# Kernel optimization log

Hardware: AMD Instinct MI355X
Metric: run time of the kernel (lower is better)

The kernel has to match this reference:

```python
import jax, jax.numpy as jnp
import numpy as np

THRESH = 0.5
LENS = 0.5
DECAY = 0.5
IN_SIZE = 8
T = 784 // IN_SIZE  # 98 timesteps
H = 1024
OUT = 10
SKIP = (2, 3, 4)
N_BATCH = 1024


@jax.custom_vjp
def act_fun(x):
    return (x > THRESH).astype(x.dtype)

def _af_fwd(x):
    return act_fun(x), x

def _af_bwd(x, g):
    return (g * (jnp.abs(x - THRESH) < LENS).astype(g.dtype),)

act_fun.defvjp(_af_fwd, _af_bwd)


def _make_mask(dim, cycle):
    base = np.array([1 if t % cycle == 0 else 0 for t in range(T)], dtype=np.int32)
    return np.stack([np.roll(base, n) for n in range(dim)])  # [dim, T]


def setup_inputs() -> dict:
    key = jax.random.key(0)
    ks = jax.random.split(key, 9)
    inp = {
        "input": jax.random.uniform(ks[0], (N_BATCH, 784), dtype=jnp.float32),
        "W1": jax.random.normal(ks[1], (H, IN_SIZE), dtype=jnp.float32) * 0.1,
        "b1": jax.random.normal(ks[2], (H,), dtype=jnp.float32) * 0.01,
        "W2": jax.random.normal(ks[3], (H, H), dtype=jnp.float32) * 0.03,
        "b2": jax.random.normal(ks[4], (H,), dtype=jnp.float32) * 0.01,
        "W3": jax.random.normal(ks[5], (H, H), dtype=jnp.float32) * 0.03,
        "b3": jax.random.normal(ks[6], (H,), dtype=jnp.float32) * 0.01,
        "W4": jax.random.normal(ks[7], (OUT, H), dtype=jnp.float32) * 0.03,
        "b4": jax.random.normal(ks[8], (OUT,), dtype=jnp.float32) * 0.01,
        "mask1": jnp.asarray(_make_mask(H, SKIP[0])),
        "mask2": jnp.asarray(_make_mask(H, SKIP[1])),
        "mask3": jnp.asarray(_make_mask(H, SKIP[2])),
    }
    return inp


def _gather_steps(x):
    # Faithful replication of the original (buggy) slicing: start = step*IN_SIZE,
    # but if start >= T - IN_SIZE the model uses the LAST IN_SIZE pixels.
    starts = np.array([s * IN_SIZE if s * IN_SIZE < T - IN_SIZE else 784 - IN_SIZE
                       for s in range(T)])
    idx = starts[:, None] + np.arange(IN_SIZE)  # [T, IN_SIZE]
    return jnp.transpose(x[:, idx], (1, 0, 2))  # [T, N, IN_SIZE]


def reference(input, W1, b1, W2, b2, W3, b3, W4, b4, mask1, mask2, mask3):
    N = input.shape[0]
    xs = _gather_steps(input)            # [T, N, IN_SIZE]
    mk1 = mask1.T                         # [T, H]
    mk2 = mask2.T
    mk3 = mask3.T

    def upd(drive, mem, spike, mk):
        mkf = mk.astype(mem.dtype)
        new_mem = mem * DECAY * (1.0 - spike) + drive
        mem = jnp.where(mk == 0, mem, new_mem)
        spike = act_fun(mem) * mkf
        return mem, spike

    zeros = lambda d: jnp.zeros((N, d), dtype=input.dtype)
    carry0 = (zeros(H), zeros(H), zeros(H), zeros(H), zeros(H), zeros(H),
              jnp.zeros((N, OUT), dtype=input.dtype), zeros(H), zeros(H), zeros(H))

    def step(carry, inp):
        m1, s1, m2, s2, m3, s3, osum, ss1, ss2, ss3 = carry
        x, k1, k2, k3 = inp
        m1, s1 = upd(x @ W1.T + b1, m1, s1, k1)
        m2, s2 = upd(s1 @ W2.T + b2, m2, s2, k2)
        m3, s3 = upd(s2 @ W3.T + b3, m3, s3, k3)
        out = s3 @ W4.T + b4
        return (m1, s1, m2, s2, m3, s3, osum + out,
                ss1 + s1, ss2 + s2, ss3 + s3), None

    carry, _ = jax.lax.scan(step, carry0, (xs, mk1, mk2, mk3))
    _, _, _, _, _, _, osum, ss1, ss2, ss3 = carry

    tw = jnp.asarray(T, dtype=input.dtype)
    outputs = osum / tw
    denom = jnp.asarray(N * H * T, dtype=input.dtype)
    layer_fr = jnp.stack([ss1.sum() / denom, ss2.sum() / denom, ss3.sum() / denom])
    hidden_spk = (ss1 / tw, ss2 / tw, ss3 / tw)
    return outputs, hidden_spk, layer_fr
```

## Files before the change

kernel.cpp:

```cpp
#include <hip/hip_runtime.h>

#define TTL 98
#define OUTD 10

typedef float f16v __attribute__((ext_vector_type(16)));
typedef short short8 __attribute__((ext_vector_type(8)));
typedef unsigned long ul2 __attribute__((ext_vector_type(2)));
typedef unsigned short ushort;

constexpr size_t MM = 1048576;
constexpr size_t OFF_OSUM = 5 * MM;
constexpr size_t OFF_XT   = OFF_OSUM + 10240;
constexpr size_t OFF_S1B  = OFF_XT + 802816;
constexpr size_t OFF_S2B  = OFF_S1B + 1605632;
constexpr size_t OFF_S1BT = OFF_S2B + 1103872;
constexpr size_t OFF_S2BT = OFF_S1BT + 1605632;
constexpr size_t OFF_W2S  = OFF_S2BT + 1103872;
constexpr size_t OFF_W3S  = OFF_W2S + 1572864;
constexpr size_t FIX_END  = OFF_W3S + 1585152;

constexpr size_t TAB_IDX2 = 0;
constexpr size_t TAB_IDX3 = 37632;
constexpr size_t TAB_RK2  = 68992;
constexpr size_t TAB_RK3  = 169344;
constexpr size_t TAB_CQ3  = 269696;
constexpr size_t TAB_L2   = 304192;
constexpr size_t TAB_L3   = 337984;

__device__ inline void split3(float w, ushort& h, ushort& m, ushort& l) {
    unsigned u = __float_as_uint(w);
    h = (ushort)(u >> 16);
    float r1 = w - __uint_as_float(u & 0xFFFF0000u);
    unsigned u1 = __float_as_uint(r1);
    m = (ushort)(u1 >> 16);
    float r2 = r1 - __uint_as_float(u1 & 0xFFFF0000u);
    l = (ushort)(__float_as_uint(r2) >> 16);
}

__device__ inline short8 expand8(unsigned x) {
    union { unsigned u[4]; short8 v; } r;
#pragma unroll
    for (int q = 0; q < 4; ++q) {
        unsigned b = x >> (2 * q);
        r.u[q] = ((b & 1u) * 0x3F80u) | ((b & 2u) ? 0x3F800000u : 0u);
    }
    return r.v;
}

__global__ __launch_bounds__(256) void kSplit(
    const float* __restrict__ W2, const float* __restrict__ W3,
    ushort* __restrict__ W2S, ushort* __restrict__ W3S)
{
    int id = blockIdx.x * 256 + threadIdx.x;
    if (id < 1048576) {
        int p = id >> 19, rem = id & 524287, i = rem >> 9, q = rem & 511;
        ushort h, m, l;
        split3(W2[i * 1024 + 2 * q + p], h, m, l);
        size_t base = (size_t)p * 524288 + (size_t)i * 512 + q;
        W2S[base] = h; W2S[base + 1048576] = m; W2S[base + 2097152] = l;
    } else {
        int id2 = id - 1048576;
        if (id2 >= 1056768) return;
        int c = id2 / 352256, rem = id2 % 352256, i = rem / 344, q = rem % 344;
        int j = c + 3 * q;
        float w = (j < 1024) ? W3[i * 1024 + j] : 0.f;
        ushort h, m, l;
        split3(w, h, m, l);
        W3S[id2] = h; W3S[id2 + 1056768] = m; W3S[id2 + 2113536] = l;
    }
}

__global__ __launch_bounds__(256) void kPrep(const float* __restrict__ input,
                                             float* __restrict__ xT)
{
    __shared__ float Ls[64][65];
    int bx = blockIdx.x, tid = threadIdx.x;
    int wt = bx >> 4, nt = bx & 15;
    int w0 = wt * 64, n0 = nt * 64;
#pragma unroll
    for (int j = 0; j < 16; ++j) {
        int flat = tid + 256 * j;
        int a = flat >> 6, c = flat & 63;
        Ls[a][c] = (w0 + c < 784) ? input[(size_t)(n0 + a) * 784 + w0 + c] : 0.f;
    }
    __syncthreads();
#pragma unroll
    for (int j = 0; j < 16; ++j) {
        int flat = tid + 256 * j;
        int ii = flat >> 6, nn = flat & 63;
        if (w0 + ii < 784) xT[(size_t)(w0 + ii) * 1024 + n0 + nn] = Ls[nn][ii];
    }
}

__global__ __launch_bounds__(256) void kL1(
    const float* __restrict__ xT, const float* __restrict__ W1,
    const float* __restrict__ b1,
    unsigned long long* __restrict__ s1bits, float* __restrict__ ss1)
{
    int tid = threadIdx.x;
    int waveId = (blockIdx.x << 2) + (tid >> 6);
    int lane = tid & 63;
    int rowg = waveId >> 4;
    int nblk = waveId & 15;
    int i0 = rowg << 2;
    int n = (nblk << 6) + lane;
    float w[4][8], bb[4], mem[4], cnt[4];
#pragma unroll
    for (int r = 0; r < 4; ++r) {
#pragma unroll
        for (int e = 0; e < 8; ++e) w[r][e] = W1[(i0 + r) * 8 + e];
        bb[r] = b1[i0 + r]; mem[r] = 0.f; cnt[r] = 0.f;
    }
    float x[8], xn[8];
#pragma unroll
    for (int e = 0; e < 8; ++e) x[e] = xT[(size_t)e * 1024 + n];
    for (int t = 0; t < TTL; ++t) {
        if (t + 1 < TTL) {
            int st1 = ((t + 1) * 8 < TTL - 8) ? (t + 1) * 8 : (784 - 8);
#pragma unroll
            for (int e = 0; e < 8; ++e) xn[e] = xT[(size_t)(st1 + e) * 1024 + n];
        }
#pragma unroll
        for (int r = 0; r < 4; ++r) {
            if (((t ^ (i0 + r)) & 1) == 0) {
                float d = bb[r];
#pragma unroll
                for (int e = 0; e < 8; ++e) d += w[r][e] * x[e];
                float m = mem[r] * 0.5f + d;
                mem[r] = m;
                bool sp = m > 0.5f;
                unsigned long long bm = __ballot(sp);
                if (lane == 0) s1bits[(size_t)(t * 512 + ((i0 + r) >> 1)) * 16 + nblk] = bm;
                if (sp) cnt[r] += 1.f;
            }
        }
#pragma unroll
        for (int e = 0; e < 8; ++e) x[e] = xn[e];
    }
#pragma unroll
    for (int r = 0; r < 4; ++r) ss1[(size_t)(i0 + r) * 1024 + n] = cnt[r];
}

__global__ __launch_bounds__(256) void kTab2(
    int* __restrict__ idx2, int* __restrict__ idx3,
    int* __restrict__ rank2, int* __restrict__ rank3, int* __restrict__ cq3)
{
    __shared__ int f2[256], f3[256];
    __shared__ int sidx2[384], sidx3[320];
    int t = blockIdx.x, tid = threadIdx.x;
    int a2[4], a3[4];
    int l2 = 0, l3 = 0;
#pragma unroll
    for (int e = 0; e < 4; ++e) {
        int i = tid * 4 + e;
        int u = (t - i) % TTL; if (u < 0) u += TTL;
        a2[e] = (u % 3 == 0); a3[e] = (u % 4 == 0);
        l2 += a2[e]; l3 += a3[e];
    }
    f2[tid] = l2; f3[tid] = l3;
    __syncthreads();
    for (int s = 1; s < 256; s <<= 1) {
        int v2 = (tid >= s) ? f2[tid - s] : 0;
        int v3 = (tid >= s) ? f3[tid - s] : 0;
        __syncthreads();
        f2[tid] += v2; f3[tid] += v3;
        __syncthreads();
    }
    int o2 = f2[tid] - l2, o3 = f3[tid] - l3;
    int c2 = f2[255], c3 = f3[255];
#pragma unroll
    for (int e = 0; e < 4; ++e) {
        int i = tid * 4 + e;
        if (a2[e]) { rank2[t * 1024 + i] = o2; sidx2[o2] = i; ++o2; }
        else rank2[t * 1024 + i] = -1;
        if (a3[e]) { rank3[t * 1024 + i] = o3; sidx3[o3] = i; ++o3; }
        else rank3[t * 1024 + i] = -1;
    }
    __syncthreads();
    for (int k = tid; k < 384; k += 256) idx2[t * 384 + k] = (k < c2) ? sidx2[k] : -1;
    for (int k = tid; k < 320; k += 256) idx3[t * 320 + k] = (k < c3) ? sidx3[k] : -1;
    for (int k = tid; k < 352; k += 256) {
        int j = (k < c2) ? sidx2[k] : 0;
        cq3[t * 352 + k] = (j % 3) * 352256 + j / 3;
    }
}

__global__ __launch_bounds__(256) void kList(
    const int* __restrict__ rank2, const int* __restrict__ rank3,
    int* __restrict__ list2, int* __restrict__ list3)
{
    int i = blockIdx.x * 256 + threadIdx.x;
    int s2 = 0, s3 = 0;
    for (int t = 0; t < TTL; ++t) {
        int rk2 = rank2[t * 1024 + i];
        if (rk2 >= 0) list2[i * 33 + s2++] = (t << 10) | rk2;
        int rk3 = rank3[t * 1024 + i];
        if (rk3 >= 0) list3[i * 25 + s3++] = (t << 10) | rk3;
    }
}

template<int K>
__global__ __launch_bounds__(256) void kXb(const unsigned* __restrict__ in,
                                           unsigned* __restrict__ out, int t0)
{
    constexpr int Kw = K / 32;
    __shared__ unsigned L[1024];
    int bx = blockIdx.x, tid = threadIdx.x;
    int tt = t0 + bx / Kw, kw = bx % Kw;
    const unsigned* ip = in + ((size_t)tt * K + kw * 32) * 32;
#pragma unroll
    for (int g = 0; g < 4; ++g) L[g * 256 + tid] = ip[g * 256 + tid];
    __syncthreads();
    unsigned* op = out + ((size_t)tt * Kw + kw) * 1024;
#pragma unroll
    for (int g = 0; g < 4; ++g) {
        int n = g * 256 + tid;
        int w = n >> 5, b = n & 31;
        unsigned acc = 0;
#pragma unroll
        for (int k = 0; k < 32; ++k) acc |= ((L[k * 32 + w] >> b) & 1u) << k;
        op[n] = acc;
    }
}

__global__ __launch_bounds__(256) void kG3A(
    const ushort* __restrict__ Ws, const int* __restrict__ idx3,
    const int* __restrict__ cq3, ushort* __restrict__ AW3, int t0)
{
    int tid = threadIdx.x, bx = blockIdx.x;
    int tloc = bx / 55, blk = bx % 55;
    int t = t0 + tloc;
    int flat = blk * 256 + tid;
    int r = flat / 44, kg = flat % 44;
    int k0 = kg * 8;
    int v = idx3[t * 320 + r];
    int i = v < 0 ? 0 : v;
    const int* cq = cq3 + t * 352 + k0;
    int c0 = cq[0], c1 = cq[1], c2 = cq[2], c3 = cq[3],
        c4 = cq[4], c5 = cq[5], c6 = cq[6], c7 = cq[7];
    size_t ia = (size_t)i * 344;
#pragma unroll
    for (int pi = 0; pi < 3; ++pi) {
        const ushort* wp = Ws + (size_t)pi * 1056768 + ia;
        union { ushort us[8]; ul2 v2; } o;
        o.us[0] = wp[c0]; o.us[1] = wp[c1]; o.us[2] = wp[c2]; o.us[3] = wp[c3];
        o.us[4] = wp[c4]; o.us[5] = wp[c5]; o.us[6] = wp[c6]; o.us[7] = wp[c7];
        *(ul2*)(AW3 + ((size_t)tloc * 3 + pi) * 112640 + (size_t)r * 352 + k0) = o.v2;
    }
}


__global__ __launch_bounds__(256) void kGM2K(
    const ushort* __restrict__ Ws, const unsigned* __restrict__ s1bT,
    const int* __restrict__ idx2, float* __restrict__ drive, int t0)
{
    __shared__ ushort As[3][64][40];
    __shared__ int iR[64];
    int tid = threadIdx.x, bx = blockIdx.x;
    int tloc = bx / 24, rem = bx % 24;
    int mt = rem >> 2, nt4 = rem & 3;
    int t = t0 + tloc;
    int p = t & 1;
    int r0 = mt * 64, n0 = nt4 * 256;
    if (tid < 64) { int v = idx2[t * 384 + r0 + tid]; iR[tid] = v < 0 ? 0 : v; }
    const ushort* Wbase = Ws + (size_t)p * 524288;
    int ar = tid >> 2, ak8 = (tid & 3) * 8;
    int wv = tid >> 6, lane = tid & 63;
    int wr = (wv >> 1) * 32, wc = (wv & 1) * 128;
    int mrow = lane & 31, kh8 = (lane >> 5) * 8;
    f16v acc[4];
#pragma unroll
    for (int j = 0; j < 4; ++j) acc[j] = (f16v)(0.f);

    for (int kc = 0; kc < 512; kc += 32) {
        __syncthreads();
        unsigned w4[4];
#pragma unroll
        for (int j = 0; j < 4; ++j)
            w4[j] = s1bT[((size_t)t * 16 + (kc >> 5)) * 1024 + n0 + wc + j * 32 + mrow];
#pragma unroll
        for (int pi = 0; pi < 3; ++pi) {
            ul2 v = *(const ul2*)(Wbase + (size_t)pi * 1048576 +
                                  (size_t)iR[ar] * 512 + kc + ak8);
            *(ul2*)&As[pi][ar][ak8] = v;
        }
        __syncthreads();
#pragma unroll
        for (int s2 = 0; s2 < 2; ++s2) {
            int kcol = s2 * 16 + kh8;
            short8 af0 = *(const short8*)&As[0][wr + mrow][kcol];
            short8 af1 = *(const short8*)&As[1][wr + mrow][kcol];
            short8 af2 = *(const short8*)&As[2][wr + mrow][kcol];
#pragma unroll
            for (int j = 0; j < 4; ++j) {
                short8 bf = expand8((w4[j] >> kcol) & 0xFFu);
                acc[j] = __builtin_amdgcn_mfma_f32_32x32x16_bf16(af2, bf, acc[j], 0, 0, 0);
                acc[j] = __builtin_amdgcn_mfma_f32_32x32x16_bf16(af1, bf, acc[j], 0, 0, 0);
                acc[j] = __builtin_amdgcn_mfma_f32_32x32x16_bf16(af0, bf, acc[j], 0, 0, 0);
            }
        }
    }
#pragma unroll
    for (int j = 0; j < 4; ++j)
#pragma unroll
        for (int reg = 0; reg < 16; ++reg) {
            int rowl = wr + (reg & 3) + 8 * (reg >> 2) + 4 * (lane >> 5);
            drive[((size_t)tloc * 384 + r0 + rowl) * 1024 + n0 + wc + j * 32 + mrow] = acc[j][reg];
        }
}

__global__ __launch_bounds__(256) void kGM3K(
    const ushort* __restrict__ AW3, const unsigned* __restrict__ s2bT,
    float* __restrict__ drive, int t0)
{
    __shared__ ushort As[3][64][40];
    int tid = threadIdx.x, bx = blockIdx.x;
    int tloc = bx / 20, rem = bx % 20;
    int mt = rem >> 2, nt4 = rem & 3;
    int t = t0 + tloc;
    int r0 = mt * 64, n0 = nt4 * 256;
    int ar = tid >> 2, ak8 = (tid & 3) * 8;
    const ushort* Ab = AW3 + (size_t)tloc * 337920 + (size_t)(r0 + ar) * 352 + ak8;
    int wv = tid >> 6, lane = tid & 63;
    int wr = (wv >> 1) * 32, wc = (wv & 1) * 128;
    int mrow = lane & 31, kh8 = (lane >> 5) * 8;
    f16v acc[4];
#pragma unroll
    for (int j = 0; j < 4; ++j) acc[j] = (f16v)(0.f);

    for (int kc = 0; kc < 352; kc += 32) {
        __syncthreads();
        unsigned w4[4];
#pragma unroll
        for (int j = 0; j < 4; ++j)
            w4[j] = s2bT[((size_t)t * 11 + (kc >> 5)) * 1024 + n0 + wc + j * 32 + mrow];
#pragma unroll
        for (int pi = 0; pi < 3; ++pi) {
            ul2 v = *(const ul2*)(Ab + (size_t)pi * 112640 + kc);
            *(ul2*)&As[pi][ar][ak8] = v;
        }
        __syncthreads();
#pragma unroll
        for (int s2 = 0; s2 < 2; ++s2) {
            int kcol = s2 * 16 + kh8;
            short8 af0 = *(const short8*)&As[0][wr + mrow][kcol];
            short8 af1 = *(const short8*)&As[1][wr + mrow][kcol];
            short8 af2 = *(const short8*)&As[2][wr + mrow][kcol];
#pragma unroll
            for (int j = 0; j < 4; ++j) {
                short8 bf = expand8((w4[j] >> kcol) & 0xFFu);
                acc[j] = __builtin_amdgcn_mfma_f32_32x32x16_bf16(af2, bf, acc[j], 0, 0, 0);
                acc[j] = __builtin_amdgcn_mfma_f32_32x32x16_bf16(af1, bf, acc[j], 0, 0, 0);
                acc[j] = __builtin_amdgcn_mfma_f32_32x32x16_bf16(af0, bf, acc[j], 0, 0, 0);
            }
        }
    }
#pragma unroll
    for (int j = 0; j < 4; ++j)
#pragma unroll
        for (int reg = 0; reg < 16; ++reg) {
            int rowl = wr + (reg & 3) + 8 * (reg >> 2) + 4 * (lane >> 5);
            drive[((size_t)tloc * 320 + r0 + rowl) * 1024 + n0 + wc + j * 32 + mrow] = acc[j][reg];
        }
}

template<int MP, int KBP, bool BITS, int NACT>
__global__ __launch_bounds__(256) void kRK(
    const float* __restrict__ drive, const float* __restrict__ bias,
    const int* __restrict__ list,
    float* __restrict__ mG, float* __restrict__ ssG,
    unsigned long long* __restrict__ bitsOut, int t0, int nt)
{
    int tid = threadIdx.x;
    int row = blockIdx.x >> 2;
    int wv  = ((blockIdx.x & 3) << 2) + (tid >> 6);
    int lane = tid & 63;
    int n = (wv << 6) + lane;
    size_t idx = (size_t)row * 1024 + n;
    float mv = mG[idx];
    float cnt = 0.f;
    float bv = bias[row];
    const int* lp = list + row * NACT;
    int t1 = t0 + nt;
    int s0 = 0;
    while (s0 < NACT && (lp[s0] >> 10) < t0) ++s0;
    int s1 = s0;
    while (s1 < NACT && (lp[s1] >> 10) < t1) ++s1;
    if (s0 < s1) {
        int v = lp[s0];
        float dn = drive[((size_t)((v >> 10) - t0) * MP + (v & 1023)) * 1024 + n];
        for (int s = s0; s < s1; ++s) {
            int vc = v;
            float dcur = dn;
            if (s + 1 < s1) {
                v = lp[s + 1];
                dn = drive[((size_t)((v >> 10) - t0) * MP + (v & 1023)) * 1024 + n];
            }
            float d = dcur + bv;
            float m = mv * 0.5f + d;
            mv = m;
            bool sp = m > 0.5f;
            if (BITS) {
                unsigned long long bm = __ballot(sp);
                if (lane == 0) bitsOut[((size_t)(vc >> 10) * KBP + (vc & 1023)) * 16 + wv] = bm;
            }
            cnt += sp ? 1.f : 0.f;
        }
    }
    mG[idx] = mv;
    ssG[idx] += cnt;
}

__global__ __launch_bounds__(256) void kTail(
    const float* __restrict__ ssBase, const float* __restrict__ W4,
    float* __restrict__ osum, float* __restrict__ out, float* __restrict__ fr)
{
    int bx = blockIdx.x, tid = threadIdx.x;
    if (bx < 768) {
        __shared__ float Ls[64][65];
        __shared__ float red[4];
        int l = bx >> 8;
        int tile = bx & 255;
        int i0 = (tile >> 4) * 64, n0 = (tile & 15) * 64;
        const float* ss = ssBase + (size_t)l * MM;
        float* o = out + 10240 + (size_t)l * MM;
        float sum = 0.f;
#pragma unroll
        for (int j = 0; j < 16; ++j) {
            int flat = tid + 256 * j;
            int a = flat >> 6, c = flat & 63;
            float v = ss[(size_t)(i0 + a) * 1024 + n0 + c];
            Ls[a][c] = v;
            sum += v;
        }
        __syncthreads();
        for (int off = 32; off > 0; off >>= 1) sum += __shfl_down(sum, off, 64);
        if ((tid & 63) == 0) red[tid >> 6] = sum;
        __syncthreads();
        if (tid == 0) {
            float s = red[0] + red[1] + red[2] + red[3];
            atomicAdd(&fr[l], s * (1.0f / (1024.0f * 1024.0f * 98.0f)));
        }
#pragma unroll
        for (int j = 0; j < 16; ++j) {
            int flat = tid + 256 * j;
            int nn = flat >> 6, ii = flat & 63;
            o[(size_t)(n0 + nn) * 1024 + i0 + ii] = Ls[ii][nn] * (1.0f / 98.0f);
        }
    } else {
        int b = bx - 768;
        int ks = b >> 4, nt = b & 15;
        int n = nt * 64 + (tid & 63);
        int og = tid >> 6;
        const float* ss3 = ssBase + (size_t)2 * MM;
        float a0 = 0.f, a1 = 0.f, a2 = 0.f;
        int k0 = ks * 256;
        for (int k = k0; k < k0 + 256; ++k) {
            float v = ss3[(size_t)k * 1024 + n];
            a0 += v * W4[og * 1024 + k];
            a1 += v * W4[(og + 4) * 1024 + k];
            if (og < 2) a2 += v * W4[(og + 8) * 1024 + k];
        }
        atomicAdd(&osum[n * OUTD + og], a0);
        atomicAdd(&osum[n * OUTD + og + 4], a1);
        if (og < 2) atomicAdd(&osum[n * OUTD + og + 8], a2);
    }
}

__global__ void kOut(const float* __restrict__ osum, const float* __restrict__ b4,
                     float* __restrict__ out)
{
    int idx = blockIdx.x * 256 + threadIdx.x;
    if (idx < 1024 * OUTD) out[idx] = osum[idx] * (1.0f / 98.0f) + b4[idx % OUTD];
}

extern "C" void kernel_launch(void* const* d_in, const int* in_sizes, int n_in,
                              void* d_out, int out_size, void* d_ws, size_t ws_size,
                              hipStream_t stream)
{
    const float* input = (const float*)d_in[0];
    const float* W1    = (const float*)d_in[1];
    const float* b1    = (const float*)d_in[2];
    const float* W2    = (const float*)d_in[3];
    const float* b2    = (const float*)d_in[4];
    const float* W3    = (const float*)d_in[5];
    const float* b3    = (const float*)d_in[6];
    const float* W4    = (const float*)d_in[7];
    const float* b4    = (const float*)d_in[8];

    float* ws = (float*)d_ws;
    float* ss1  = ws;
    float* ss2  = ws + MM;
    float* ss3  = ws + 2 * MM;
    float* m2   = ws + 3 * MM;
    float* m3   = ws + 4 * MM;
    float* osum = ws + OFF_OSUM;
    float* xT   = ws + OFF_XT;
    int*   tabs = (int*)(ws + OFF_XT);
    int* idx2  = tabs + TAB_IDX2;
    int* idx3  = tabs + TAB_IDX3;
    int* rank2 = tabs + TAB_RK2;
    int* rank3 = tabs + TAB_RK3;
    int* cq3   = tabs + TAB_CQ3;
    int* list2 = tabs + TAB_L2;
    int* list3 = tabs + TAB_L3;
    unsigned int* s1b  = (unsigned int*)(ws + OFF_S1B);
    unsigned int* s2b  = (unsigned int*)(ws + OFF_S2B);
    unsigned int* s1bT = (unsigned int*)(ws + OFF_S1BT);
    unsigned int* s2bT = (unsigned int*)(ws + OFF_S2BT);
    ushort* W2S = (ushort*)(ws + OFF_W2S);
    ushort* W3S = (ushort*)(ws + OFF_W3S);
    float* out  = (float*)d_out;

    size_t availF = ws_size / sizeof(float);
    constexpr size_t PER_T = 84480 + 384 * 1024 + 320 * 1024;
    int tc = 14;
    const int cands[7] = {98, 66, 49, 40, 33, 25, 14};
    for (int ci = 0; ci < 7; ++ci) {
        if (FIX_END + (size_t)cands[ci] * PER_T <= availF) { tc = cands[ci]; break; }
    }
    ushort* AW3 = (ushort*)(ws + FIX_END);
    float* drv2 = ws + FIX_END + (size_t)tc * 84480;
    float* drv3 = drv2 + (size_t)tc * 384 * 1024;

    hipMemsetAsync(ws, 0, (5 * MM + 10240) * sizeof(float), stream);
    hipMemsetAsync(s2b, 0, 1103872 * sizeof(unsigned int), stream);
    hipMemsetAsync(out + 3155968, 0, 3 * sizeof(float), stream);

    kSplit<<<8224, 256, 0, stream>>>(W2, W3, W2S, W3S);
    kPrep<<<208, 256, 0, stream>>>(input, xT);
    kL1<<<1024, 256, 0, stream>>>(xT, W1, b1, (unsigned long long*)s1b, ss1);
    kTab2<<<98, 256, 0, stream>>>(idx2, idx3, rank2, rank3, cq3);
    kList<<<4, 256, 0, stream>>>(rank2, rank3, list2, list3);
    kXb<512><<<1568, 256, 0, stream>>>(s1b, s1bT, 0);

    for (int t0 = 0; t0 < TTL; t0 += tc) {
        int nt = (TTL - t0 < tc) ? (TTL - t0) : tc;
        kGM2K<<<nt * 24, 256, 0, stream>>>(W2S, s1bT, idx2, drv2, t0);
        kRK<384, 352, true, 33><<<4096, 256, 0, stream>>>(drv2, b2, list2, m2, ss2,
                                                          (unsigned long long*)s2b, t0, nt);
        kXb<352><<<nt * 11, 256, 0, stream>>>(s2b, s2bT, t0);
        kG3A<<<nt * 55, 256, 0, stream>>>(W3S, idx3, cq3, AW3, t0);
        kGM3K<<<nt * 20, 256, 0, stream>>>(AW3, s2bT, drv3, t0);
        kRK<320, 0, false, 25><<<4096, 256, 0, stream>>>(drv3, b3, list3, m3, ss3,
                                                         nullptr, t0, nt);
    }

    kTail<<<832, 256, 0, stream>>>(ss1, W4, osum, out, out + 3155968);
    kOut<<<40, 256, 0, stream>>>(osum, b4, out);
}
```

Measured before the change: 614.4 us.

## Prefetch next K-chunk into registers and remap warp tiles in spike GEMMs

```diff
diff --git a/kernel.cpp b/kernel.cpp
--- a/kernel.cpp
+++ b/kernel.cpp
@@ -255,58 +255,76 @@
     const int* __restrict__ idx2, float* __restrict__ drive, int t0)
 {
     __shared__ ushort As[3][64][40];
-    __shared__ int iR[64];
     int tid = threadIdx.x, bx = blockIdx.x;
     int tloc = bx / 24, rem = bx % 24;
     int mt = rem >> 2, nt4 = rem & 3;
     int t = t0 + tloc;
     int p = t & 1;
     int r0 = mt * 64, n0 = nt4 * 256;
-    if (tid < 64) { int v = idx2[t * 384 + r0 + tid]; iR[tid] = v < 0 ? 0 : v; }
-    const ushort* Wbase = Ws + (size_t)p * 524288;
     int ar = tid >> 2, ak8 = (tid & 3) * 8;
+    int vR = idx2[t * 384 + r0 + ar];
+    const ushort* Wrow = Ws + (size_t)p * 524288 + (size_t)(vR < 0 ? 0 : vR) * 512 + ak8;
     int wv = tid >> 6, lane = tid & 63;
-    int wr = (wv >> 1) * 32, wc = (wv & 1) * 128;
     int mrow = lane & 31, kh8 = (lane >> 5) * 8;
-    f16v acc[4];
-#pragma unroll
-    for (int j = 0; j < 4; ++j) acc[j] = (f16v)(0.f);
+    int nb = n0 + wv * 64 + mrow;
+    f16v acc[2][2];
+#pragma unroll
+    for (int a = 0; a < 2; ++a)
+#pragma unroll
+        for (int b = 0; b < 2; ++b) acc[a][b] = (f16v)(0.f);
+
+    ul2 pre[3];
+#pragma unroll
+    for (int pi = 0; pi < 3; ++pi) pre[pi] = *(const ul2*)(Wrow + (size_t)pi * 1048576);
+    unsigned w4c[2];
+#pragma unroll
+    for (int jj = 0; jj < 2; ++jj) w4c[jj] = s1bT[(size_t)t * 16 * 1024 + nb + jj * 32];
 
     for (int kc = 0; kc < 512; kc += 32) {
-        __syncthreads();
-        unsigned w4[4];
-#pragma unroll
-        for (int j = 0; j < 4; ++j)
-            w4[j] = s1bT[((size_t)t * 16 + (kc >> 5)) * 1024 + n0 + wc + j * 32 + mrow];
-#pragma unroll
-        for (int pi = 0; pi < 3; ++pi) {
-            ul2 v = *(const ul2*)(Wbase + (size_t)pi * 1048576 +
-                                  (size_t)iR[ar] * 512 + kc + ak8);
-            *(ul2*)&As[pi][ar][ak8] = v;
-        }
-        __syncthreads();
+#pragma unroll
+        for (int pi = 0; pi < 3; ++pi) *(ul2*)&As[pi][ar][ak8] = pre[pi];
+        __syncthreads();
+        ul2 nxt[3]; unsigned w4n[2];
+        if (kc + 32 < 512) {
+#pragma unroll
+            for (int jj = 0; jj < 2; ++jj)
+                w4n[jj] = s1bT[((size_t)t * 16 + ((kc + 32) >> 5)) * 1024 + nb + jj * 32];
+#pragma unroll
+            for (int pi = 0; pi < 3; ++pi)
+                nxt[pi] = *(const ul2*)(Wrow + (size_t)pi * 1048576 + kc + 32);
+        }
 #pragma unroll
         for (int s2 = 0; s2 < 2; ++s2) {
             int kcol = s2 * 16 + kh8;
-            short8 af0 = *(const short8*)&As[0][wr + mrow][kcol];
-            short8 af1 = *(const short8*)&As[1][wr + mrow][kcol];
-            short8 af2 = *(const short8*)&As[2][wr + mrow][kcol];
-#pragma unroll
-            for (int j = 0; j < 4; ++j) {
-                short8 bf = expand8((w4[j] >> kcol) & 0xFFu);
-                acc[j] = __builtin_amdgcn_mfma_f32_32x32x16_bf16(af2, bf, acc[j], 0, 0, 0);
-                acc[j] = __builtin_amdgcn_mfma_f32_32x32x16_bf16(af1, bf, acc[j], 0, 0, 0);
-                acc[j] = __builtin_amdgcn_mfma_f32_32x32x16_bf16(af0, bf, acc[j], 0, 0, 0);
-            }
-        }
-    }
-#pragma unroll
-    for (int j = 0; j < 4; ++j)
-#pragma unroll
-        for (int reg = 0; reg < 16; ++reg) {
-            int rowl = wr + (reg & 3) + 8 * (reg >> 2) + 4 * (lane >> 5);
-            drive[((size_t)tloc * 384 + r0 + rowl) * 1024 + n0 + wc + j * 32 + mrow] = acc[j][reg];
-        }
+            short8 bf[2];
+#pragma unroll
+            for (int jj = 0; jj < 2; ++jj) bf[jj] = expand8((w4c[jj] >> kcol) & 0xFFu);
+#pragma unroll
+            for (int wr2 = 0; wr2 < 2; ++wr2) {
+                short8 af0 = *(const short8*)&As[0][wr2 * 32 + mrow][kcol];
+                short8 af1 = *(const short8*)&As[1][wr2 * 32 + mrow][kcol];
+                short8 af2 = *(const short8*)&As[2][wr2 * 32 + mrow][kcol];
+#pragma unroll
+                for (int jj = 0; jj < 2; ++jj) {
+                    acc[wr2][jj] = __builtin_amdgcn_mfma_f32_32x32x16_bf16(af2, bf[jj], acc[wr2][jj], 0, 0, 0);
+                    acc[wr2][jj] = __builtin_amdgcn_mfma_f32_32x32x16_bf16(af1, bf[jj], acc[wr2][jj], 0, 0, 0);
+                    acc[wr2][jj] = __builtin_amdgcn_mfma_f32_32x32x16_bf16(af0, bf[jj], acc[wr2][jj], 0, 0, 0);
+                }
+            }
+        }
+        __syncthreads();
+        pre[0] = nxt[0]; pre[1] = nxt[1]; pre[2] = nxt[2];
+        w4c[0] = w4n[0]; w4c[1] = w4n[1];
+    }
+#pragma unroll
+    for (int wr2 = 0; wr2 < 2; ++wr2)
+#pragma unroll
+        for (int jj = 0; jj < 2; ++jj)
+#pragma unroll
+            for (int reg = 0; reg < 16; ++reg) {
+                int rowl = r0 + wr2 * 32 + (reg & 3) + 8 * (reg >> 2) + 4 * (lane >> 5);
+                drive[((size_t)tloc * 384 + rowl) * 1024 + nb + jj * 32] = acc[wr2][jj][reg];
+            }
 }
 
 __global__ __launch_bounds__(256) void kGM3K(
@@ -322,46 +340,66 @@
     int ar = tid >> 2, ak8 = (tid & 3) * 8;
     const ushort* Ab = AW3 + (size_t)tloc * 337920 + (size_t)(r0 + ar) * 352 + ak8;
     int wv = tid >> 6, lane = tid & 63;
-    int wr = (wv >> 1) * 32, wc = (wv & 1) * 128;
     int mrow = lane & 31, kh8 = (lane >> 5) * 8;
-    f16v acc[4];
-#pragma unroll
-    for (int j = 0; j < 4; ++j) acc[j] = (f16v)(0.f);
+    int nb = n0 + wv * 64 + mrow;
+    f16v acc[2][2];
+#pragma unroll
+    for (int a = 0; a < 2; ++a)
+#pragma unroll
+        for (int b = 0; b < 2; ++b) acc[a][b] = (f16v)(0.f);
+
+    ul2 pre[3];
+#pragma unroll
+    for (int pi = 0; pi < 3; ++pi) pre[pi] = *(const ul2*)(Ab + (size_t)pi * 112640);
+    unsigned w4c[2];
+#pragma unroll
+    for (int jj = 0; jj < 2; ++jj) w4c[jj] = s2bT[(size_t)t * 11 * 1024 + nb + jj * 32];
 
     for (int kc = 0; kc < 352; kc += 32) {
-        __syncthreads();
-        unsigned w4[4];
-#pragma unroll
-        for (int j = 0; j < 4; ++j)
-            w4[j] = s2bT[((size_t)t * 11 + (kc >> 5)) * 1024 + n0 + wc + j * 32 + mrow];
-#pragma unroll
-        for (int pi = 0; pi < 3; ++pi) {
-            ul2 v = *(const ul2*)(Ab + (size_t)pi * 112640 + kc);
-            *(ul2*)&As[pi][ar][ak8] = v;
-        }
-        __syncthreads();
+#pragma unroll
+        for (int pi = 0; pi < 3; ++pi) *(ul2*)&As[pi][ar][ak8] = pre[pi];
+        __syncthreads();
+        ul2 nxt[3]; unsigned w4n[2];
+        if (kc + 32 < 352) {
+#pragma unroll
+            for (int jj = 0; jj < 2; ++jj)
+                w4n[jj] = s2bT[((size_t)t * 11 + ((kc + 32) >> 5)) * 1024 + nb + jj * 32];
+#pragma unroll
+            for (int pi = 0; pi < 3; ++pi)
+                nxt[pi] = *(const ul2*)(Ab + (size_t)pi * 112640 + kc + 32);
+        }
 #pragma unroll
         for (int s2 = 0; s2 < 2; ++s2) {
             int kcol = s2 * 16 + kh8;
-            short8 af0 = *(const short8*)&As[0][wr + mrow][kcol];
-            short8 af1 = *(const short8*)&As[1][wr + mrow][kcol];
-            short8 af2 = *(const short8*)&As[2][wr + mrow][kcol];
-#pragma unroll
-            for (int j = 0; j < 4; ++j) {
-                short8 bf = expand8((w4[j] >> kcol) & 0xFFu);
-                acc[j] = __builtin_amdgcn_mfma_f32_32x32x16_bf16(af2, bf, acc[j], 0, 0, 0);
-                acc[j] = __builtin_amdgcn_mfma_f32_32x32x16_bf16(af1, bf, acc[j], 0, 0, 0);
-                acc[j] = __builtin_amdgcn_mfma_f32_32x32x16_bf16(af0, bf, acc[j], 0, 0, 0);
-            }
-        }
-    }
-#pragma unroll
-    for (int j = 0; j < 4; ++j)
-#pragma unroll
-        for (int reg = 0; reg < 16; ++reg) {
-            int rowl = wr + (reg & 3) + 8 * (reg >> 2) + 4 * (lane >> 5);
-            drive[((size_t)tloc * 320 + r0 + rowl) * 1024 + n0 + wc + j * 32 + mrow] = acc[j][reg];
-        }
+            short8 bf[2];
+#pragma unroll
+            for (int jj = 0; jj < 2; ++jj) bf[jj] = expand8((w4c[jj] >> kcol) & 0xFFu);
+#pragma unroll
+            for (int wr2 = 0; wr2 < 2; ++wr2) {
+                short8 af0 = *(const short8*)&As[0][wr2 * 32 + mrow][kcol];
+                short8 af1 = *(const short8*)&As[1][wr2 * 32 + mrow][kcol];
+                short8 af2 = *(const short8*)&As[2][wr2 * 32 + mrow][kcol];
+#pragma unroll
+                for (int jj = 0; jj < 2; ++jj) {
+                    acc[wr2][jj] = __builtin_amdgcn_mfma_f32_32x32x16_bf16(af2, bf[jj], acc[wr2][jj], 0, 0, 0);
+                    acc[wr2][jj] = __builtin_amdgcn_mfma_f32_32x32x16_bf16(af1, bf[jj], acc[wr2][jj], 0, 0, 0);
+                    acc[wr2][jj] = __builtin_amdgcn_mfma_f32_32x32x16_bf16(af0, bf[jj], acc[wr2][jj], 0, 0, 0);
+                }
+            }
+        }
+        __syncthreads();
+        pre[0] = nxt[0]; pre[1] = nxt[1]; pre[2] = nxt[2];
+        w4c[0] = w4n[0]; w4c[1] = w4n[1];
+    }
+#pragma unroll
+    for (int wr2 = 0; wr2 < 2; ++wr2)
+#pragma unroll
+        for (int jj = 0; jj < 2; ++jj)
+#pragma unroll
+            for (int reg = 0; reg < 16; ++reg) {
+                int rowl = r0 + wr2 * 32 + (reg & 3) + 8 * (reg >> 2) + 4 * (lane >> 5);
+                drive[((size_t)tloc * 320 + rowl) * 1024 + nb + jj * 32] = acc[wr2][jj][reg];
+            }
 }
 
 template<int MP, int KBP, bool BITS, int NACT>
```

Result: no change. 614.3 us (-0.0%).
